# Kernel optimization log

Measured on AMD Instinct MI355X. Metric: run time of the kernel, lower is better.

The kernel has to match this reference:

```python
import jax, jax.numpy as jnp
import numpy as np


def setup_inputs() -> dict:
    key = jax.random.key(0)
    B, C, A, P, N = 4, 1, 180, 384, 256
    sinogram = jax.random.normal(key, (B, C, A, P), dtype=jnp.float32)
    # projection angles uniformly covering [0, pi)
    thetas = jnp.linspace(0.0, np.pi, A, endpoint=False).astype(jnp.float32)
    # uniformly spaced detector positions centered at 0, unit spacing
    positions = jnp.arange(P, dtype=jnp.float32) - (P - 1) / 2.0
    return {"sinogram": sinogram, "thetas": thetas, "positions": positions, "image_size": N}


def reference(sinogram, thetas, positions, image_size):
    """Radon backprojection: image[y,x] = sum_a interp(sinogram[a], x*cos+y*sin)."""
    B, C, A, P = sinogram.shape
    N = image_size
    # pixel-center coordinates, image centered at origin (y axis pointing up)
    c = jnp.arange(N, dtype=sinogram.dtype) - (N - 1) / 2.0
    xs = c[None, :]          # [1, N]
    ys = -c[:, None]         # [N, 1]
    cos = jnp.cos(thetas)[:, None, None]  # [A, 1, 1]
    sin = jnp.sin(thetas)[:, None, None]
    t = xs[None] * cos + ys[None] * sin   # [A, N, N] detector coordinate per (angle, pixel)
    # fractional index into the (uniform) detector position grid
    dp = positions[1] - positions[0]
    f = (t - positions[0]) / dp           # [A, N, N]
    i0 = jnp.floor(f)
    w = f - i0                            # linear interpolation weight
    valid = (i0 >= 0) & (i0 <= P - 2)     # rays falling inside the detector
    i0c = jnp.clip(i0, 0, P - 2).astype(jnp.int32)
    idx = i0c.reshape(A, N * N)[None, None]          # [1, 1, A, N*N]
    v0 = jnp.take_along_axis(sinogram, idx, axis=3)  # [B, C, A, N*N]
    v1 = jnp.take_along_axis(sinogram, idx + 1, axis=3)
    wf = w.reshape(A, N * N)[None, None]
    vm = valid.reshape(A, N * N)[None, None]
    val = jnp.where(vm, v0 * (1.0 - wf) + v1 * wf, 0.0)
    return val.sum(axis=2).reshape(B, C, N, N)
```

## Files before the change

### kernel.cpp

```cpp
#include <hip/hip_runtime.h>
#include <hip/hip_fp16.h>
#include <cmath>


#define AGROUPS 8

typedef __fp16 half2v __attribute__((ext_vector_type(2)));

__device__ __forceinline__ half2v as_h2(unsigned u) {
    union { unsigned u; half2v h; } x; x.u = u; return x.h;
}

__global__ __launch_bounds__(256) void radon_pack(
    const float* __restrict__ sino,
    const float* __restrict__ thetas,
    const float* __restrict__ positions,
    uint4* __restrict__ packed,
    float2* __restrict__ trig,
    int A, int P, int PES, int bstride)
{
    const int gidx = blockIdx.x * 256 + threadIdx.x;
    const int a = gidx / PES;
    const int j = gidx - a * PES;
    if (a >= A) return;

    const float p0     = positions[0];
    const float inv_dp = 1.0f / (positions[1] - p0);
    if (j == 0) {
        float th = thetas[a];
        trig[a] = make_float2(cosf(th) * inv_dp, sinf(th) * inv_dp);
        if (a == 0) trig[A] = make_float2(-p0 * inv_dp, 0.0f);
    }

    uint4 e = make_uint4(0, 0, 0, 0);
    if (j >= 1 && j <= P - 1) {
        const float* s = sino + (size_t)a * P + (j - 1);
        unsigned* ep = (unsigned*)&e;
#pragma unroll
        for (int b = 0; b < 4; ++b) {
            float2 v = *(const float2*)(s + (size_t)b * bstride);
            half2v h = __builtin_amdgcn_cvt_pkrtz(v.x, v.y);
            union { half2v h; unsigned u; } cvt; cvt.h = h;
            ep[b] = cvt.u;
        }
    }
    packed[(size_t)a * PES + j] = e;
}

__global__ __launch_bounds__(1024, 8) void radon_gather_red(
    const uint4* __restrict__ packed,
    const float2* __restrict__ trig,
    float* __restrict__ out,
    int A, int P, int PES, int N, int chunk)
{
    __shared__ float red[AGROUPS][128][4];

    const int tid = threadIdx.x;
    const int nn  = N * N;
    const int g   = tid >> 7;
    const int p   = tid & 127;

    const int hf = p >> 6;
    const int l  = p & 63;
    const int lx = l & 15;
    const int ly = l >> 4;
    const int tilesx = N >> 5;
    const int bx = blockIdx.x % tilesx;
    const int by = blockIdx.x / tilesx;
    const int x  = (bx << 5) + (hf << 4) + lx;
    const int y  = (by << 2) + ly;

    const int a0 = g * chunk;
    const int a1 = min(A, a0 + chunk);

    const float half_ = (float)(N - 1) * 0.5f;
    const float cx = (float)x - half_;
    const float cy = half_ - (float)y;
    const float q0 = trig[A].x;

    float acc0 = 0.f, acc1 = 0.f, acc2 = 0.f, acc3 = 0.f;

#pragma unroll 4
    for (int a = a0; a < a1; ++a) {
        float2 t  = trig[a];
        float f   = fmaf(cx, t.x, fmaf(cy, t.y, q0));
        float i0f = floorf(f);
        float w_  = f - i0f;
        int   i0  = (int)i0f;
        int   j   = min(max(i0, -1), P - 1) + 1;

        half2v w2 = __builtin_amdgcn_cvt_pkrtz(1.0f - w_, w_);
        uint4 e = packed[a * PES + j];
        acc0 = __builtin_amdgcn_fdot2(as_h2(e.x), w2, acc0, false);
        acc1 = __builtin_amdgcn_fdot2(as_h2(e.y), w2, acc1, false);
        acc2 = __builtin_amdgcn_fdot2(as_h2(e.z), w2, acc2, false);
        acc3 = __builtin_amdgcn_fdot2(as_h2(e.w), w2, acc3, false);
    }

    red[g][p][0] = acc0;
    red[g][p][1] = acc1;
    red[g][p][2] = acc2;
    red[g][p][3] = acc3;
    __syncthreads();

    if (tid < 512) {
        const int b2 = tid >> 7;
        const int p2 = tid & 127;
        float s = 0.0f;
#pragma unroll
        for (int gg = 0; gg < AGROUPS; ++gg) s += red[gg][p2][b2];

        const int hf2 = p2 >> 6;
        const int l2  = p2 & 63;
        const int x2  = (bx << 5) + (hf2 << 4) + (l2 & 15);
        const int y2  = (by << 2) + (l2 >> 4);
        out[(size_t)b2 * nn + y2 * N + x2] = s;
    }
}

__global__ __launch_bounds__(256) void radon_direct_kernel(
    const float* __restrict__ sino,
    const float* __restrict__ thetas,
    const float* __restrict__ positions,
    float* __restrict__ out,
    int A, int P, int N, int BC)
{
    const int nn  = N * N;
    const int pix = blockIdx.x * blockDim.x + threadIdx.x;
    if (pix >= nn) return;
    const float p0     = positions[0];
    const float inv_dp = 1.0f / (positions[1] - p0);
    const int x = pix % N;
    const int y = pix / N;
    const float half = (float)(N - 1) * 0.5f;
    const float cx = (float)x - half;
    const float cy = half - (float)y;
    for (int b = 0; b < BC; ++b) {
        float acc = 0.0f;
        for (int a = 0; a < A; ++a) {
            float th = thetas[a];
            float f  = (cx * cosf(th) + cy * sinf(th) - p0) * inv_dp;
            float i0f = floorf(f);
            int i0 = (int)i0f;
            float w = f - i0f;
            float m = (i0 >= 0 && i0 <= P - 2) ? 1.0f : 0.0f;
            int ic = min(max(i0, 0), P - 2);
            const float* row = sino + ((size_t)b * A + a) * P + ic;
            acc = fmaf(m, fmaf(w, row[1] - row[0], row[0]), acc);
        }
        out[(size_t)b * nn + pix] = acc;
    }
}

extern "C" void kernel_launch(void* const* d_in, const int* in_sizes, int n_in,
                              void* d_out, int out_size, void* d_ws, size_t ws_size,
                              hipStream_t stream) {
    const float* sino      = (const float*)d_in[0];
    const float* thetas    = (const float*)d_in[1];
    const float* positions = (const float*)d_in[2];
    float* out             = (float*)d_out;

    const int A  = in_sizes[1];
    const int P  = in_sizes[2];
    const int BC = in_sizes[0] / (A * P);
    const int N  = (int)lroundf(sqrtf((float)(out_size / BC)));
    const int nn = N * N;
    const int bstride = A * P;

    const int PES   = (P + 2 + 63) & ~63;
    const int chunk = (A + AGROUPS - 1) / AGROUPS;

    const size_t packed_bytes = (size_t)A * PES * sizeof(uint4);
    const size_t trig_bytes   = (size_t)(A + 1) * sizeof(float2);
    const size_t need = packed_bytes + trig_bytes;

    const bool fast = (BC == 4) && (A <= 1024) && (P >= 2)
                   && (N % 32 == 0) && (ws_size >= need);

    if (fast) {
        uint4*  packed = (uint4*)d_ws;
        float2* trig   = (float2*)((char*)d_ws + packed_bytes);

        dim3 block(256);
        dim3 gpack(((unsigned)(A * PES) + 255) / 256);
        radon_pack<<<gpack, block, 0, stream>>>(
            sino, thetas, positions, packed, trig, A, P, PES, bstride);

        dim3 gblock(1024);
        dim3 ggat((N / 32) * (N / 4));
        radon_gather_red<<<ggat, gblock, 0, stream>>>(
            packed, trig, out, A, P, PES, N, chunk);
    } else {
        dim3 block(256);
        dim3 grid((nn + 255) / 256);
        radon_direct_kernel<<<grid, block, 0, stream>>>(
            sino, thetas, positions, out, A, P, N, BC);
    }
}
```

Before: 72.47 us.

## Fuse pack step into gather kernel and read fp32 sinogram directly

Result: slower. 86.27 us (+19.0%).

```diff
diff --git a/kernel.cpp b/kernel.cpp
--- a/kernel.cpp
+++ b/kernel.cpp
@@ -5,61 +5,31 @@
 
 #define AGROUPS 8
 
-typedef __fp16 half2v __attribute__((ext_vector_type(2)));
-
-__device__ __forceinline__ half2v as_h2(unsigned u) {
-    union { unsigned u; half2v h; } x; x.u = u; return x.h;
-}
-
-__global__ __launch_bounds__(256) void radon_pack(
+__global__ __launch_bounds__(1024, 8) void radon_fused(
     const float* __restrict__ sino,
     const float* __restrict__ thetas,
     const float* __restrict__ positions,
-    uint4* __restrict__ packed,
-    float2* __restrict__ trig,
-    int A, int P, int PES, int bstride)
+    float* __restrict__ out,
+    int A, int P, int N, int chunk)
 {
-    const int gidx = blockIdx.x * 256 + threadIdx.x;
-    const int a = gidx / PES;
-    const int j = gidx - a * PES;
-    if (a >= A) return;
+    __shared__ float red[AGROUPS][128][4];
+    __shared__ float2 trig_s[1024];
+
+    const int tid = threadIdx.x;
 
     const float p0     = positions[0];
     const float inv_dp = 1.0f / (positions[1] - p0);
-    if (j == 0) {
-        float th = thetas[a];
-        trig[a] = make_float2(cosf(th) * inv_dp, sinf(th) * inv_dp);
-        if (a == 0) trig[A] = make_float2(-p0 * inv_dp, 0.0f);
+    if (tid < A) {
+        float th = thetas[tid];
+        trig_s[tid] = make_float2(cosf(th) * inv_dp, sinf(th) * inv_dp);
     }
+    __syncthreads();
 
-    uint4 e = make_uint4(0, 0, 0, 0);
-    if (j >= 1 && j <= P - 1) {
-        const float* s = sino + (size_t)a * P + (j - 1);
-        unsigned* ep = (unsigned*)&e;
-#pragma unroll
-        for (int b = 0; b < 4; ++b) {
-            float2 v = *(const float2*)(s + (size_t)b * bstride);
-            half2v h = __builtin_amdgcn_cvt_pkrtz(v.x, v.y);
-            union { half2v h; unsigned u; } cvt; cvt.h = h;
-            ep[b] = cvt.u;
-        }
-    }
-    packed[(size_t)a * PES + j] = e;
-}
+    const float q0 = -p0 * inv_dp;
 
-__global__ __launch_bounds__(1024, 8) void radon_gather_red(
-    const uint4* __restrict__ packed,
-    const float2* __restrict__ trig,
-    float* __restrict__ out,
-    int A, int P, int PES, int N, int chunk)
-{
-    __shared__ float red[AGROUPS][128][4];
-
-    const int tid = threadIdx.x;
-    const int nn  = N * N;
-    const int g   = tid >> 7;
-    const int p   = tid & 127;
-
+    const int nn = N * N;
+    const int g  = tid >> 7;
+    const int p  = tid & 127;
     const int hf = p >> 6;
     const int l  = p & 63;
     const int lx = l & 15;
@@ -76,25 +46,35 @@
     const float half_ = (float)(N - 1) * 0.5f;
     const float cx = (float)x - half_;
     const float cy = half_ - (float)y;
-    const float q0 = trig[A].x;
+
+    const int AP = A * P;
+    const float* __restrict__ s0 = sino;
+    const float* __restrict__ s1 = sino + AP;
+    const float* __restrict__ s2 = sino + 2 * AP;
+    const float* __restrict__ s3 = sino + 3 * AP;
 
     float acc0 = 0.f, acc1 = 0.f, acc2 = 0.f, acc3 = 0.f;
 
 #pragma unroll 4
     for (int a = a0; a < a1; ++a) {
-        float2 t  = trig[a];
+        float2 t  = trig_s[a];
         float f   = fmaf(cx, t.x, fmaf(cy, t.y, q0));
         float i0f = floorf(f);
-        float w_  = f - i0f;
+        float w   = f - i0f;
         int   i0  = (int)i0f;
-        int   j   = min(max(i0, -1), P - 1) + 1;
+        float m   = (i0 >= 0 && i0 <= P - 2) ? 1.0f : 0.0f;
+        int   ic  = min(max(i0, 0), P - 2);
+        const int off = a * P + ic;
 
-        half2v w2 = __builtin_amdgcn_cvt_pkrtz(1.0f - w_, w_);
-        uint4 e = packed[a * PES + j];
-        acc0 = __builtin_amdgcn_fdot2(as_h2(e.x), w2, acc0, false);
-        acc1 = __builtin_amdgcn_fdot2(as_h2(e.y), w2, acc1, false);
-        acc2 = __builtin_amdgcn_fdot2(as_h2(e.z), w2, acc2, false);
-        acc3 = __builtin_amdgcn_fdot2(as_h2(e.w), w2, acc3, false);
+        float2 v0 = *(const float2*)(s0 + off);
+        float2 v1 = *(const float2*)(s1 + off);
+        float2 v2 = *(const float2*)(s2 + off);
+        float2 v3 = *(const float2*)(s3 + off);
+
+        acc0 = fmaf(m, fmaf(w, v0.y - v0.x, v0.x), acc0);
+        acc1 = fmaf(m, fmaf(w, v1.y - v1.x, v1.x), acc1);
+        acc2 = fmaf(m, fmaf(w, v2.y - v2.x, v2.x), acc2);
+        acc3 = fmaf(m, fmaf(w, v3.y - v3.x, v3.x), acc3);
     }
 
     red[g][p][0] = acc0;
@@ -165,31 +145,16 @@
     const int BC = in_sizes[0] / (A * P);
     const int N  = (int)lroundf(sqrtf((float)(out_size / BC)));
     const int nn = N * N;
-    const int bstride = A * P;
 
-    const int PES   = (P + 2 + 63) & ~63;
     const int chunk = (A + AGROUPS - 1) / AGROUPS;
 
-    const size_t packed_bytes = (size_t)A * PES * sizeof(uint4);
-    const size_t trig_bytes   = (size_t)(A + 1) * sizeof(float2);
-    const size_t need = packed_bytes + trig_bytes;
-
-    const bool fast = (BC == 4) && (A <= 1024) && (P >= 2)
-                   && (N % 32 == 0) && (ws_size >= need);
+    const bool fast = (BC == 4) && (A <= 1024) && (P >= 2) && (N % 32 == 0);
 
     if (fast) {
-        uint4*  packed = (uint4*)d_ws;
-        float2* trig   = (float2*)((char*)d_ws + packed_bytes);
-
-        dim3 block(256);
-        dim3 gpack(((unsigned)(A * PES) + 255) / 256);
-        radon_pack<<<gpack, block, 0, stream>>>(
-            sino, thetas, positions, packed, trig, A, P, PES, bstride);
-
         dim3 gblock(1024);
         dim3 ggat((N / 32) * (N / 4));
-        radon_gather_red<<<ggat, gblock, 0, stream>>>(
-            packed, trig, out, A, P, PES, N, chunk);
+        radon_fused<<<ggat, gblock, 0, stream>>>(
+            sino, thetas, positions, out, A, P, N, chunk);
     } else {
         dim3 block(256);
         dim3 grid((nn + 255) / 256);
```
